# Performance work log

Hardware: AMD Instinct MI355X
Metric: run time of the kernel (lower is better)

The kernel has to match this reference:

```python
import jax, jax.numpy as jnp
import numpy as np

N = 100000      # n_nodes
E = 1600000     # n_edges (avg degree 16)
IN, HID, OUT = 128, 128, 64
P = 0.5         # dropout prob


def setup_inputs() -> dict:
    key = jax.random.key(0)
    k = jax.random.split(key, 6)
    x = jax.random.normal(k[0], (N, IN), dtype=jnp.float32)
    edge_index = jax.random.randint(k[1], (2, E), 0, N, dtype=jnp.int32)
    W1 = jax.random.normal(k[2], (IN, HID), dtype=jnp.float32) / np.sqrt(IN)
    b1 = jnp.zeros((HID,), dtype=jnp.float32)
    W2 = jax.random.normal(k[3], (HID, OUT), dtype=jnp.float32) / np.sqrt(HID)
    b2 = jnp.zeros((OUT,), dtype=jnp.float32)
    return {"x": x, "edge_index": edge_index, "W1": W1, "b1": b1, "W2": W2, "b2": b2}


def gcn_conv(x, W, b, src, dst, num_nodes):
    """PyG GCNConv: add self-loops, symmetric D^-1/2 A D^-1/2 normalization,
    linear transform then scatter-add aggregation at destination nodes."""
    loop = jnp.arange(num_nodes, dtype=src.dtype)
    s = jnp.concatenate([src, loop])  # [E+N]
    d = jnp.concatenate([dst, loop])
    deg = jax.ops.segment_sum(jnp.ones_like(d, dtype=x.dtype), d, num_segments=num_nodes)
    dinv = jnp.where(deg > 0, jax.lax.rsqrt(jnp.maximum(deg, 1e-12)), 0.0)
    norm = dinv[s] * dinv[d]                     # [E+N]
    h = x @ W                                    # [N, F_out] (transform first: cheaper)
    msg = h[s] * norm[:, None]                   # gather + scale
    out = jax.ops.segment_sum(msg, d, num_segments=num_nodes)  # scatter-add
    return out + b


def reference(x, edge_index, W1, b1, W2, b2):
    src, dst = edge_index[0], edge_index[1]
    h = jax.nn.relu(gcn_conv(x, W1, b1, src, dst, N))
    # F.dropout(training=True) with a fixed key for determinism
    keep = jax.random.bernoulli(jax.random.key(42), 1.0 - P, h.shape)
    h = jnp.where(keep, h / (1.0 - P), 0.0)
    return gcn_conv(h, W2, b2, src, dst, N)
```

## Files before the change

### kernel.cpp

```cpp
#include <hip/hip_runtime.h>


constexpr int NN    = 100000;
constexpr int NE    = 1600000;
constexpr int SCAN_CHUNK = 2048;
constexpr int NSCAN = (NN + SCAN_CHUNK - 1) / SCAN_CHUNK;

typedef __attribute__((ext_vector_type(8))) short short8v;
typedef __attribute__((ext_vector_type(4))) float f32x4;

__device__ __forceinline__ float bf2f(unsigned short u) {
  return __uint_as_float(((unsigned)u) << 16);
}
__device__ __forceinline__ unsigned short f2bf(float f) {
  unsigned x = __float_as_uint(f);
  return (unsigned short)((x + 0x7fffu + ((x >> 16) & 1u)) >> 16);
}
__device__ __forceinline__ float lo16(unsigned p) { return bf2f((unsigned short)(p & 0xffffu)); }
__device__ __forceinline__ float hi16(unsigned p) { return bf2f((unsigned short)(p >> 16)); }

__device__ __forceinline__ unsigned tf_rotl(unsigned x, int r) {
  return (x << r) | (x >> (32 - r));
}

__device__ __forceinline__ void threefry2x32_0_42(unsigned in0, unsigned in1,
                                                  unsigned& o0, unsigned& o1) {
  const unsigned K0 = 0u, K1 = 42u;
  const unsigned K2 = 0x1BD11BDAu ^ K0 ^ K1;
  unsigned x0 = in0 + K0, x1 = in1 + K1;
#define TFR(r) { x0 += x1; x1 = tf_rotl(x1, r); x1 ^= x0; }
  TFR(13) TFR(15) TFR(26) TFR(6)
  x0 += K1; x1 += K2 + 1u;
  TFR(17) TFR(29) TFR(16) TFR(24)
  x0 += K2; x1 += K0 + 2u;
  TFR(13) TFR(15) TFR(26) TFR(6)
  x0 += K0; x1 += K1 + 3u;
  TFR(17) TFR(29) TFR(16) TFR(24)
  x0 += K1; x1 += K2 + 4u;
  TFR(13) TFR(15) TFR(26) TFR(6)
  x0 += K2; x1 += K0 + 5u;
#undef TFR
  o0 = x0; o1 = x1;
}

__device__ __forceinline__ bool dropout_keep(unsigned i) {
  unsigned a, b; threefry2x32_0_42(0u, i, a, b);
  return ((a ^ b) >> 31) == 0u;
}


__global__ __launch_bounds__(256) void hist_kernel(const int* __restrict__ dst,
                                                   int* __restrict__ cnt) {
  int e = blockIdx.x * 256 + threadIdx.x;
  if (e < NE) atomicAdd(&cnt[dst[e]], 1);
}

__global__ __launch_bounds__(256) void scan1_kernel(const int* __restrict__ cnt,
                                                    int* __restrict__ off,
                                                    int* __restrict__ blksum,
                                                    float* __restrict__ dinv) {
  __shared__ int tsum[256];
  const int base = blockIdx.x * SCAN_CHUNK + threadIdx.x * 8;
  int v[8]; int s = 0;
#pragma unroll
  for (int j = 0; j < 8; j++) {
    int idx = base + j;
    v[j] = (idx < NN) ? cnt[idx] : 0;
    s += v[j];
    if (idx < NN) dinv[idx] = rsqrtf((float)v[j] + 1.0f);
  }
  tsum[threadIdx.x] = s;
  __syncthreads();
  for (int d = 1; d < 256; d <<= 1) {
    int t = (threadIdx.x >= d) ? tsum[threadIdx.x - d] : 0;
    __syncthreads();
    tsum[threadIdx.x] += t;
    __syncthreads();
  }
  int run = tsum[threadIdx.x] - s;
  if (threadIdx.x == 255) blksum[blockIdx.x] = tsum[255];
#pragma unroll
  for (int j = 0; j < 8; j++) {
    int idx = base + j;
    if (idx < NN) { off[idx] = run; run += v[j]; }
  }
}

__global__ void scan2_kernel(int* __restrict__ blksum, int* __restrict__ off) {
  if (threadIdx.x == 0) {
    int run = 0;
    for (int i = 0; i < NSCAN; i++) { int t = blksum[i]; blksum[i] = run; run += t; }
    off[NN] = NE;
  }
}

__global__ __launch_bounds__(256) void scan3_kernel(int* __restrict__ off,
                                                    const int* __restrict__ blksum) {
  const int base = blockIdx.x * SCAN_CHUNK + threadIdx.x * 8;
  const int add = blksum[blockIdx.x];
#pragma unroll
  for (int j = 0; j < 8; j++) {
    int idx = base + j;
    if (idx < NN) off[idx] += add;
  }
}

__global__ __launch_bounds__(256) void permute_kernel(const int* __restrict__ src,
                                                      const int* __restrict__ dst,
                                                      const int* __restrict__ off,
                                                      int* __restrict__ cur,
                                                      const float* __restrict__ dinv,
                                                      int* __restrict__ srcs,
                                                      float* __restrict__ nrms) {
  int e = blockIdx.x * 256 + threadIdx.x;
  if (e >= NE) return;
  int d = dst[e], s = src[e];
  int p = off[d] + atomicAdd(&cur[d], 1);
  srcs[p] = s;
  nrms[p] = dinv[s] * dinv[d];
}


template <int C, bool BF16_IN>
__global__ __launch_bounds__(256) void gemm_mfma_kernel(const void* __restrict__ Xv,
                                                        const float* __restrict__ W,
                                                        unsigned short* __restrict__ H,
                                                        int nrows) {
  constexpr int STR = 136;
  __shared__ unsigned short Xs[64 * STR];
  __shared__ unsigned short Wt[C * STR];
  const int row0 = blockIdx.x * 64;
  const int nr = min(64, nrows - row0);
  const int tid = threadIdx.x;

  for (int t = tid; t < C * 64; t += 256) {
    int n = t % C, kk = t / C;
    unsigned pk = ((unsigned)f2bf(W[(2 * kk + 1) * C + n]) << 16) | f2bf(W[(2 * kk) * C + n]);
    *(unsigned*)&Wt[n * STR + 2 * kk] = pk;
  }
  if (BF16_IN) {
    const unsigned* X = (const unsigned*)Xv + (size_t)row0 * 64;
    for (int t = tid; t < 64 * 64; t += 256) {
      int r = t >> 6, kp = t & 63;
      unsigned p = (r < nr) ? X[r * 64 + kp] : 0u;
      *(unsigned*)&Xs[r * STR + 2 * kp] = p;
    }
  } else {
    const float* X = (const float*)Xv + (size_t)row0 * 128;
    for (int t = tid; t < 64 * 64; t += 256) {
      int r = t >> 6, kp = t & 63;
      unsigned p = 0u;
      if (r < nr) {
        float2 v = *(const float2*)&X[r * 128 + 2 * kp];
        p = ((unsigned)f2bf(v.y) << 16) | f2bf(v.x);
      }
      *(unsigned*)&Xs[r * STR + 2 * kp] = p;
    }
  }
  __syncthreads();

  const int w  = tid >> 6;
  const int l  = tid & 63;
  const int lr = l & 15;
  const int lk = l >> 4;
  constexpr int NT = C / 16;

  f32x4 acc[NT];
#pragma unroll
  for (int nt = 0; nt < NT; nt++) acc[nt] = (f32x4){0.f, 0.f, 0.f, 0.f};

  short8v afr[4];
  const int arow = w * 16 + lr;
#pragma unroll
  for (int ks = 0; ks < 4; ks++)
    afr[ks] = *(const short8v*)&Xs[arow * STR + ks * 32 + lk * 8];

#pragma unroll
  for (int nt = 0; nt < NT; nt++) {
    const int ncol = nt * 16 + lr;
#pragma unroll
    for (int ks = 0; ks < 4; ks++) {
      short8v bfr = *(const short8v*)&Wt[ncol * STR + ks * 32 + lk * 8];
      acc[nt] = __builtin_amdgcn_mfma_f32_16x16x32_bf16(afr[ks], bfr, acc[nt], 0, 0, 0);
    }
  }

#pragma unroll
  for (int nt = 0; nt < NT; nt++) {
#pragma unroll
    for (int r = 0; r < 4; r++) {
      int row = w * 16 + lk * 4 + r;
      if (row < nr) H[(size_t)(row0 + row) * C + nt * 16 + lr] = f2bf(acc[nt][r]);
    }
  }
}


__global__ __launch_bounds__(256) void gather1_kernel(const int* __restrict__ off,
                                                      const int* __restrict__ srcs,
                                                      const float* __restrict__ nrms,
                                                      const unsigned* __restrict__ hb,
                                                      const float* __restrict__ dinv,
                                                      const float* __restrict__ b1,
                                                      unsigned* __restrict__ hd) {
  int nid = blockIdx.x * 4 + (threadIdx.x >> 6);
  if (nid >= NN) return;
  int c = threadIdx.x & 63;
  float di = dinv[nid];
  unsigned hp = hb[(size_t)nid * 64 + c];
  float a0 = lo16(hp) * di * di;
  float a1 = hi16(hp) * di * di;
  int beg = off[nid], end = off[nid + 1];
  int e = beg;
  for (; e + 4 <= end; e += 4) {
    int s0 = srcs[e], s1 = srcs[e + 1], s2 = srcs[e + 2], s3 = srcs[e + 3];
    float w0 = nrms[e], w1 = nrms[e + 1], w2 = nrms[e + 2], w3 = nrms[e + 3];
    unsigned p0 = hb[(size_t)s0 * 64 + c];
    unsigned p1 = hb[(size_t)s1 * 64 + c];
    unsigned p2 = hb[(size_t)s2 * 64 + c];
    unsigned p3 = hb[(size_t)s3 * 64 + c];
    a0 = fmaf(lo16(p0), w0, a0); a1 = fmaf(hi16(p0), w0, a1);
    a0 = fmaf(lo16(p1), w1, a0); a1 = fmaf(hi16(p1), w1, a1);
    a0 = fmaf(lo16(p2), w2, a0); a1 = fmaf(hi16(p2), w2, a1);
    a0 = fmaf(lo16(p3), w3, a0); a1 = fmaf(hi16(p3), w3, a1);
  }
  for (; e < end; e++) {
    int s = srcs[e];
    float w = nrms[e];
    unsigned p = hb[(size_t)s * 64 + c];
    a0 = fmaf(lo16(p), w, a0);
    a1 = fmaf(hi16(p), w, a1);
  }
  a0 += b1[2 * c];
  a1 += b1[2 * c + 1];
  a0 = fmaxf(a0, 0.f);
  a1 = fmaxf(a1, 0.f);
  unsigned i0 = (unsigned)nid * 128u + 2u * (unsigned)c;
  a0 = dropout_keep(i0)      ? 2.f * a0 : 0.f;
  a1 = dropout_keep(i0 + 1u) ? 2.f * a1 : 0.f;
  hd[(size_t)nid * 64 + c] = ((unsigned)f2bf(a1) << 16) | f2bf(a0);
}


__global__ __launch_bounds__(256) void gather2_kernel(const int* __restrict__ off,
                                                      const int* __restrict__ srcs,
                                                      const float* __restrict__ nrms,
                                                      const unsigned short* __restrict__ h2b,
                                                      const float* __restrict__ dinv,
                                                      const float* __restrict__ b2,
                                                      float* __restrict__ out) {
  int nid = blockIdx.x * 4 + (threadIdx.x >> 6);
  if (nid >= NN) return;
  int c = threadIdx.x & 63;
  float di = dinv[nid];
  float acc = bf2f(h2b[(size_t)nid * 64 + c]) * di * di;
  int beg = off[nid], end = off[nid + 1];
  int e = beg;
  for (; e + 4 <= end; e += 4) {
    int s0 = srcs[e], s1 = srcs[e + 1], s2 = srcs[e + 2], s3 = srcs[e + 3];
    float w0 = nrms[e], w1 = nrms[e + 1], w2 = nrms[e + 2], w3 = nrms[e + 3];
    float v0 = bf2f(h2b[(size_t)s0 * 64 + c]);
    float v1 = bf2f(h2b[(size_t)s1 * 64 + c]);
    float v2 = bf2f(h2b[(size_t)s2 * 64 + c]);
    float v3 = bf2f(h2b[(size_t)s3 * 64 + c]);
    acc = fmaf(v0, w0, acc);
    acc = fmaf(v1, w1, acc);
    acc = fmaf(v2, w2, acc);
    acc = fmaf(v3, w3, acc);
  }
  for (; e < end; e++) {
    acc = fmaf(bf2f(h2b[(size_t)srcs[e] * 64 + c]), nrms[e], acc);
  }
  out[(size_t)nid * 64 + c] = acc + b2[c];
}


extern "C" void kernel_launch(void* const* d_in, const int* in_sizes, int n_in,
                              void* d_out, int out_size, void* d_ws, size_t ws_size,
                              hipStream_t stream) {
  const float* x  = (const float*)d_in[0];
  const int*   ei = (const int*)d_in[1];
  const float* W1 = (const float*)d_in[2];
  const float* b1 = (const float*)d_in[3];
  const float* W2 = (const float*)d_in[4];
  const float* b2 = (const float*)d_in[5];
  float* out = (float*)d_out;

  const int* src = ei;
  const int* dst = ei + NE;

  char* p = (char*)d_ws;
  auto take = [&](size_t bytes) { char* q = p; p += (bytes + 15) & ~size_t(15); return q; };
  int*      cnt    = (int*)take(sizeof(int) * NN);
  int*      off    = (int*)take(sizeof(int) * (NN + 1));
  int*      blksum = (int*)take(sizeof(int) * NSCAN);
  float*    dinv   = (float*)take(sizeof(float) * NN);
  int*      srcs   = (int*)take(sizeof(int) * NE);
  float*    nrms   = (float*)take(sizeof(float) * NE);
  unsigned* hb     = (unsigned*)take(sizeof(unsigned) * (size_t)NN * 64);
  unsigned* hd     = (unsigned*)take(sizeof(unsigned) * (size_t)NN * 64);
  unsigned* h2b    = (unsigned*)take(sizeof(unsigned) * (size_t)NN * 32);

  hipMemsetAsync(cnt, 0, sizeof(int) * NN, stream);
  hist_kernel<<<(NE + 255) / 256, 256, 0, stream>>>(dst, cnt);
  scan1_kernel<<<NSCAN, 256, 0, stream>>>(cnt, off, blksum, dinv);
  scan2_kernel<<<1, 64, 0, stream>>>(blksum, off);
  scan3_kernel<<<NSCAN, 256, 0, stream>>>(off, blksum);
  hipMemsetAsync(cnt, 0, sizeof(int) * NN, stream);
  permute_kernel<<<(NE + 255) / 256, 256, 0, stream>>>(src, dst, off, cnt, dinv, srcs, nrms);

  gemm_mfma_kernel<128, false><<<(NN + 63) / 64, 256, 0, stream>>>(
      x, W1, (unsigned short*)hb, NN);
  gather1_kernel<<<(NN + 3) / 4, 256, 0, stream>>>(off, srcs, nrms, hb, dinv, b1, hd);

  gemm_mfma_kernel<64, true><<<(NN + 63) / 64, 256, 0, stream>>>(
      hd, W2, (unsigned short*)h2b, NN);
  gather2_kernel<<<(NN + 3) / 4, 256, 0, stream>>>(
      off, srcs, nrms, (const unsigned short*)h2b, dinv, b2, out);
}
```

Measured before the change: 484.3 us.

## Drop per-edge norm array, recompute weights from dinv in gathers, unroll by 8

The permute step no longer stores a per-edge normalization array. It seeds its cursor by copying the offsets, so the atomicAdd returns the final position directly. Both gather kernels now compute each edge weight as dinv[src]*dinv[dst] on the fly and unroll their edge loops by 8 to keep more loads in flight. This removes writing and reading a 1.6M-float array, at the cost of an extra random dinv gather per edge, which should mostly hit in cache.

New measurement: 513.9 us. 6.1% more time.

```diff
diff --git a/kernel.cpp b/kernel.cpp
--- a/kernel.cpp
+++ b/kernel.cpp
@@ -107,17 +107,12 @@
 
 __global__ __launch_bounds__(256) void permute_kernel(const int* __restrict__ src,
                                                       const int* __restrict__ dst,
-                                                      const int* __restrict__ off,
                                                       int* __restrict__ cur,
-                                                      const float* __restrict__ dinv,
-                                                      int* __restrict__ srcs,
-                                                      float* __restrict__ nrms) {
+                                                      int* __restrict__ srcs) {
   int e = blockIdx.x * 256 + threadIdx.x;
   if (e >= NE) return;
-  int d = dst[e], s = src[e];
-  int p = off[d] + atomicAdd(&cur[d], 1);
-  srcs[p] = s;
-  nrms[p] = dinv[s] * dinv[d];
+  int p = atomicAdd(&cur[dst[e]], 1);
+  srcs[p] = src[e];
 }
 
 
@@ -198,7 +193,6 @@
 
 __global__ __launch_bounds__(256) void gather1_kernel(const int* __restrict__ off,
                                                       const int* __restrict__ srcs,
-                                                      const float* __restrict__ nrms,
                                                       const unsigned* __restrict__ hb,
                                                       const float* __restrict__ dinv,
                                                       const float* __restrict__ b1,
@@ -212,21 +206,23 @@
   float a1 = hi16(hp) * di * di;
   int beg = off[nid], end = off[nid + 1];
   int e = beg;
-  for (; e + 4 <= end; e += 4) {
-    int s0 = srcs[e], s1 = srcs[e + 1], s2 = srcs[e + 2], s3 = srcs[e + 3];
-    float w0 = nrms[e], w1 = nrms[e + 1], w2 = nrms[e + 2], w3 = nrms[e + 3];
-    unsigned p0 = hb[(size_t)s0 * 64 + c];
-    unsigned p1 = hb[(size_t)s1 * 64 + c];
-    unsigned p2 = hb[(size_t)s2 * 64 + c];
-    unsigned p3 = hb[(size_t)s3 * 64 + c];
-    a0 = fmaf(lo16(p0), w0, a0); a1 = fmaf(hi16(p0), w0, a1);
-    a0 = fmaf(lo16(p1), w1, a0); a1 = fmaf(hi16(p1), w1, a1);
-    a0 = fmaf(lo16(p2), w2, a0); a1 = fmaf(hi16(p2), w2, a1);
-    a0 = fmaf(lo16(p3), w3, a0); a1 = fmaf(hi16(p3), w3, a1);
+  for (; e + 8 <= end; e += 8) {
+    int s[8]; float w[8]; unsigned p[8];
+#pragma unroll
+    for (int j = 0; j < 8; j++) s[j] = srcs[e + j];
+#pragma unroll
+    for (int j = 0; j < 8; j++) w[j] = dinv[s[j]] * di;
+#pragma unroll
+    for (int j = 0; j < 8; j++) p[j] = hb[(size_t)s[j] * 64 + c];
+#pragma unroll
+    for (int j = 0; j < 8; j++) {
+      a0 = fmaf(lo16(p[j]), w[j], a0);
+      a1 = fmaf(hi16(p[j]), w[j], a1);
+    }
   }
   for (; e < end; e++) {
     int s = srcs[e];
-    float w = nrms[e];
+    float w = dinv[s] * di;
     unsigned p = hb[(size_t)s * 64 + c];
     a0 = fmaf(lo16(p), w, a0);
     a1 = fmaf(hi16(p), w, a1);
@@ -244,7 +240,6 @@
 
 __global__ __launch_bounds__(256) void gather2_kernel(const int* __restrict__ off,
                                                       const int* __restrict__ srcs,
-                                                      const float* __restrict__ nrms,
                                                       const unsigned short* __restrict__ h2b,
                                                       const float* __restrict__ dinv,
                                                       const float* __restrict__ b2,
@@ -256,20 +251,20 @@
   float acc = bf2f(h2b[(size_t)nid * 64 + c]) * di * di;
   int beg = off[nid], end = off[nid + 1];
   int e = beg;
-  for (; e + 4 <= end; e += 4) {
-    int s0 = srcs[e], s1 = srcs[e + 1], s2 = srcs[e + 2], s3 = srcs[e + 3];
-    float w0 = nrms[e], w1 = nrms[e + 1], w2 = nrms[e + 2], w3 = nrms[e + 3];
-    float v0 = bf2f(h2b[(size_t)s0 * 64 + c]);
-    float v1 = bf2f(h2b[(size_t)s1 * 64 + c]);
-    float v2 = bf2f(h2b[(size_t)s2 * 64 + c]);
-    float v3 = bf2f(h2b[(size_t)s3 * 64 + c]);
-    acc = fmaf(v0, w0, acc);
-    acc = fmaf(v1, w1, acc);
-    acc = fmaf(v2, w2, acc);
-    acc = fmaf(v3, w3, acc);
+  for (; e + 8 <= end; e += 8) {
+    int s[8]; float w[8]; float v[8];
+#pragma unroll
+    for (int j = 0; j < 8; j++) s[j] = srcs[e + j];
+#pragma unroll
+    for (int j = 0; j < 8; j++) w[j] = dinv[s[j]] * di;
+#pragma unroll
+    for (int j = 0; j < 8; j++) v[j] = bf2f(h2b[(size_t)s[j] * 64 + c]);
+#pragma unroll
+    for (int j = 0; j < 8; j++) acc = fmaf(v[j], w[j], acc);
   }
   for (; e < end; e++) {
-    acc = fmaf(bf2f(h2b[(size_t)srcs[e] * 64 + c]), nrms[e], acc);
+    int s = srcs[e];
+    acc = fmaf(bf2f(h2b[(size_t)s * 64 + c]), dinv[s] * di, acc);
   }
   out[(size_t)nid * 64 + c] = acc + b2[c];
 }
@@ -292,11 +287,11 @@
   char* p = (char*)d_ws;
   auto take = [&](size_t bytes) { char* q = p; p += (bytes + 15) & ~size_t(15); return q; };
   int*      cnt    = (int*)take(sizeof(int) * NN);
+  int*      cur    = (int*)take(sizeof(int) * NN);
   int*      off    = (int*)take(sizeof(int) * (NN + 1));
   int*      blksum = (int*)take(sizeof(int) * NSCAN);
   float*    dinv   = (float*)take(sizeof(float) * NN);
   int*      srcs   = (int*)take(sizeof(int) * NE);
-  float*    nrms   = (float*)take(sizeof(float) * NE);
   unsigned* hb     = (unsigned*)take(sizeof(unsigned) * (size_t)NN * 64);
   unsigned* hd     = (unsigned*)take(sizeof(unsigned) * (size_t)NN * 64);
   unsigned* h2b    = (unsigned*)take(sizeof(unsigned) * (size_t)NN * 32);
@@ -306,15 +301,15 @@
   scan1_kernel<<<NSCAN, 256, 0, stream>>>(cnt, off, blksum, dinv);
   scan2_kernel<<<1, 64, 0, stream>>>(blksum, off);
   scan3_kernel<<<NSCAN, 256, 0, stream>>>(off, blksum);
-  hipMemsetAsync(cnt, 0, sizeof(int) * NN, stream);
-  permute_kernel<<<(NE + 255) / 256, 256, 0, stream>>>(src, dst, off, cnt, dinv, srcs, nrms);
+  hipMemcpyAsync(cur, off, sizeof(int) * NN, hipMemcpyDeviceToDevice, stream);
+  permute_kernel<<<(NE + 255) / 256, 256, 0, stream>>>(src, dst, cur, srcs);
 
   gemm_mfma_kernel<128, false><<<(NN + 63) / 64, 256, 0, stream>>>(
       x, W1, (unsigned short*)hb, NN);
-  gather1_kernel<<<(NN + 3) / 4, 256, 0, stream>>>(off, srcs, nrms, hb, dinv, b1, hd);
+  gather1_kernel<<<(NN + 3) / 4, 256, 0, stream>>>(off, srcs, hb, dinv, b1, hd);
 
   gemm_mfma_kernel<64, true><<<(NN + 63) / 64, 256, 0, stream>>>(
       hd, W2, (unsigned short*)h2b, NN);
   gather2_kernel<<<(NN + 3) / 4, 256, 0, stream>>>(
-      off, srcs, nrms, (const unsigned short*)h2b, dinv, b2, out);
-}
+      off, srcs, (const unsigned short*)h2b, dinv, b2, out);
+}
```
